# Performance work log

Measured on AMD Instinct MI355X. Metric: run time of the kernel, lower is better.

The kernel has to match this reference:

```python
import jax, jax.numpy as jnp
import numpy as np

N_ITER = 5          # n_iterations
EPS_VAR = 1e-6      # added to var (both in update_likelihoods and after M-step)
EPS = 1e-7          # division guard in M-step


def setup_inputs() -> dict:
    key = jax.random.key(0)
    B, N, K, F = 8, 80000, 5, 20
    k1, k2 = jax.random.split(key)
    data = jax.random.normal(k1, (B, N, F), dtype=jnp.float32)
    # initialize_parameters: means are randomly sampled data points
    idx = jax.random.randint(k2, (B, K), 0, N)
    means = jnp.take_along_axis(data, idx[:, :, None], axis=1)          # [B,K,F]
    variance = jnp.ones((B, K, F), dtype=jnp.float32)                    # covariance_init=1.0
    prior = jnp.full((B, K), 1.0 / K, dtype=jnp.float32)
    return {"data": data, "means": means, "variance": variance, "prior": prior}


def _log_likelihoods(data, means, var, pi):
    # data [B,N,F], means/var [B,K,F], pi [B,K] -> [B,K,N]
    inv_cov = 1.0 / (var + EPS_VAR)                                       # [B,K,F]
    diff = data[:, None, :, :] - means[:, :, None, :]                     # [B,K,N,F]
    maha = jnp.einsum('bknf,bkf->bkn', diff * diff, inv_cov)              # bmm in torch
    coeff = -0.5 * jnp.log(2.0 * np.pi * var).sum(axis=-1)                # [B,K]
    return jnp.log(pi)[:, :, None] + coeff[:, :, None] - 0.5 * maha


def _posteriors(log_lik):
    # stable softmax over the cluster dim (dim=1), identical to update_posteriors
    return jax.nn.softmax(log_lik, axis=1)


def _m_step(post, data):
    # post [B,K,N], data [B,N,F]; weights == 1.0 branch of update_parameters
    n = data.shape[1]
    sizes = post.sum(axis=2, keepdims=True)                               # [B,K,1] cluster sizes
    pi = sizes[..., 0] / n                                                # [B,K]
    pi = pi / jnp.maximum(jnp.abs(pi).sum(axis=-1, keepdims=True), 1e-12) # L1 normalize
    means = jnp.einsum('bkn,bnf->bkf', post, data) / (sizes + EPS)        # [B,K,F]
    diff = data[:, None, :, :] - means[:, :, None, :]                     # [B,K,N,F]
    var = jnp.einsum('bkn,bknf->bkf', post, diff * diff) / (sizes + EPS)
    return means, var, pi


def reference(data, means, variance, prior):
    var, pi = variance, prior
    for _ in range(N_ITER):
        ll = _log_likelihoods(data, means, var, pi)
        post = _posteriors(ll)
        means, var, pi = _m_step(post, data)
        var = var + EPS_VAR
    ll = _log_likelihoods(data, means, var, pi)
    post = _posteriors(ll)
    # outputs permuted to [B, N, K] as in forward()
    return (jnp.transpose(ll, (0, 2, 1)), jnp.transpose(post, (0, 2, 1)), means, var, pi)
```

## Files before the change

kernel.cpp:

```cpp
#include <hip/hip_runtime.h>
#include <math.h>

#define BB 8
#define NPTS 80000
#define KK 5
#define FF 20
#define GG 128
#define TILE 64
#define NTILES (NPTS / TILE)
#define PSTRIDE 48

#define WS_CM 0
#define WS_CV 800
#define WS_CP 1600
#define WS_A  1640
#define WS_D  1680
#define WS_E  2480

__device__ __forceinline__ void make_coefs(const float* __restrict__ means,
                                           const float* __restrict__ var,
                                           const float* __restrict__ pi,
                                           float* __restrict__ A, float* __restrict__ D,
                                           float* __restrict__ E, int t) {
    if (t < BB * KK) {
        float sumlog = 0.f, summ2 = 0.f;
        for (int f = 0; f < FF; ++f) {
            float v = var[t * FF + f];
            float m = means[t * FF + f];
            float ic = 1.f / (v + 1e-6f);
            sumlog += logf(6.283185307179586f * v);
            summ2  += ic * m * m;
            D[t * FF + f] = ic * m;
            E[t * FF + f] = -0.5f * ic;
        }
        A[t] = logf(pi[t]) - 0.5f * sumlog - 0.5f * summ2;
    }
}

__global__ void prepare_kernel(const float* __restrict__ means, const float* __restrict__ var,
                               const float* __restrict__ pi, float* __restrict__ ws) {
    make_coefs(means, var, pi, ws + WS_A, ws + WS_D, ws + WS_E, (int)threadIdx.x);
}

template <bool WRITE_OUT>
__global__ __launch_bounds__(320) void estep_kernel(const float* __restrict__ data,
                                                    const float* __restrict__ ws,
                                                    float* __restrict__ partials,
                                                    float* __restrict__ out_ll,
                                                    float* __restrict__ out_post) {
    __shared__ float xs[FF][TILE + 1];
    __shared__ float lls[KK][TILE];

    const int b    = blockIdx.x / GG;
    const int g    = blockIdx.x % GG;
    const int tid  = threadIdx.x;
    const int w    = __builtin_amdgcn_readfirstlane(tid >> 6);
    const int lane = tid & 63;
    const int sp   = (tid * 4) / FF;
    const int sf   = (tid * 4) % FF;

    const float* A = ws + WS_A;
    const float* D = ws + WS_D;
    const float* E = ws + WS_E;

    const float Ak = A[b * KK + w];
    float dk[FF], ek[FF];
#pragma unroll
    for (int f = 0; f < FF; ++f) {
        dk[f] = D[(b * KK + w) * FF + f];
        ek[f] = E[(b * KK + w) * FF + f];
    }

    float s0 = 0.f, s1[FF], s2[FF];
    if (!WRITE_OUT) {
#pragma unroll
        for (int f = 0; f < FF; ++f) { s1[f] = 0.f; s2[f] = 0.f; }
    }

    const float* dbase = data + (size_t)b * NPTS * FF;

    float4 v = ((const float4*)(dbase + (size_t)g * TILE * FF))[tid];
    for (int t = g; t < NTILES; t += GG) {
        const int tn = t + GG;
        float4 vn = v;
        if (tn < NTILES) vn = ((const float4*)(dbase + (size_t)tn * TILE * FF))[tid];

        xs[sf][sp] = v.x; xs[sf + 1][sp] = v.y; xs[sf + 2][sp] = v.z; xs[sf + 3][sp] = v.w;
        __syncthreads();

        float x[FF];
        float z = Ak;
#pragma unroll
        for (int f = 0; f < FF; ++f) {
            x[f] = xs[f][lane];
            z += x[f] * fmaf(ek[f], x[f], dk[f]);
        }
        lls[w][lane] = z;
        __syncthreads();

        float l0 = lls[0][lane], l1 = lls[1][lane], l2 = lls[2][lane],
              l3 = lls[3][lane], l4 = lls[4][lane];
        float mx = fmaxf(fmaxf(fmaxf(l0, l1), fmaxf(l2, l3)), l4);
        float e0 = __expf(l0 - mx), e1 = __expf(l1 - mx), e2 = __expf(l2 - mx),
              e3 = __expf(l3 - mx), e4 = __expf(l4 - mx);
        float inv = 1.f / (e0 + e1 + e2 + e3 + e4);
        float ew  = (w == 0) ? e0 : (w == 1) ? e1 : (w == 2) ? e2 : (w == 3) ? e3 : e4;
        float post = ew * inv;

        if (WRITE_OUT) {
            size_t o = ((size_t)b * NPTS + (size_t)t * TILE + lane) * KK + w;
            out_ll[o]   = z;
            out_post[o] = post;
        } else {
            s0 += post;
#pragma unroll
            for (int f = 0; f < FF; ++f) {
                float px = post * x[f];
                s1[f] += px;
                s2[f] += px * x[f];
            }
        }
        v = vn;
    }

    if (!WRITE_OUT) {
#pragma unroll
        for (int off = 32; off > 0; off >>= 1) {
            s0 += __shfl_down(s0, off);
#pragma unroll
            for (int f = 0; f < FF; ++f) {
                s1[f] += __shfl_down(s1[f], off);
                s2[f] += __shfl_down(s2[f], off);
            }
        }
        if (lane == 0) {
            float* row = partials + ((size_t)(b * KK + w) * GG + g) * PSTRIDE;
#pragma unroll
            for (int f = 0; f < FF; ++f) { row[f] = s1[f]; row[FF + f] = s2[f]; }
            row[2 * FF] = s0;
        }
    }
}

__global__ __launch_bounds__(320) void update_kernel(const float* __restrict__ partials,
                                                     float* __restrict__ ws,
                                                     float* __restrict__ om,
                                                     float* __restrict__ ov,
                                                     float* __restrict__ op,
                                                     int write_params) {
    __shared__ float s0s[KK];
    const int b    = blockIdx.x;
    const int tid  = threadIdx.x;
    const int w    = tid >> 6;
    const int lane = tid & 63;
    const int bk   = b * KK + w;

    float sv = 0.f;
    if (lane < PSTRIDE) {
        const float* base = partials + (size_t)bk * GG * PSTRIDE + lane;
        for (int gg = 0; gg < GG; ++gg) sv += base[(size_t)gg * PSTRIDE];
    }
    float s0  = __shfl(sv, 2 * FF);
    float den = s0 + 1e-7f;
    float m   = sv / den;
    float s2f = __shfl(sv, FF + (lane % FF));
    float var = (s2f - 2.f * m * sv + m * m * s0) / den + 1e-6f;

    float* cm = ws + WS_CM; float* cv = ws + WS_CV; float* cp = ws + WS_CP;
    if (lane < FF) {
        cm[bk * FF + lane] = m;
        cv[bk * FF + lane] = var;
        if (write_params) { om[bk * FF + lane] = m; ov[bk * FF + lane] = var; }
    }

    if (lane == 0) s0s[w] = s0;
    __syncthreads();
    float tot = s0s[0] + s0s[1] + s0s[2] + s0s[3] + s0s[4];
    float pr  = (s0 / (float)NPTS) / fmaxf(tot / (float)NPTS, 1e-12f);
    if (lane == 0) {
        cp[bk] = pr;
        if (write_params) op[bk] = pr;
    }

    float ic = 1.f / (var + 1e-6f);
    if (lane < FF) {
        (ws + WS_D)[bk * FF + lane] = ic * m;
        (ws + WS_E)[bk * FF + lane] = -0.5f * ic;
    }
    float t1 = (lane < FF) ? logf(6.283185307179586f * var) : 0.f;
    float t2 = (lane < FF) ? ic * m * m : 0.f;
#pragma unroll
    for (int off = 1; off < 64; off <<= 1) {
        t1 += __shfl_xor(t1, off);
        t2 += __shfl_xor(t2, off);
    }
    if (lane == 0)
        (ws + WS_A)[bk] = logf(pr) - 0.5f * t1 - 0.5f * t2;
}

extern "C" void kernel_launch(void* const* d_in, const int* in_sizes, int n_in,
                              void* d_out, int out_size, void* d_ws, size_t ws_size,
                              hipStream_t stream) {
    const float* data     = (const float*)d_in[0];
    const float* in_means = (const float*)d_in[1];
    const float* in_var   = (const float*)d_in[2];
    const float* in_pi    = (const float*)d_in[3];
    float* ws  = (float*)d_ws;
    float* out = (float*)d_out;

    float* out_ll   = out;
    float* out_post = out + (size_t)BB * NPTS * KK;
    float* om       = out + 2 * (size_t)BB * NPTS * KK;
    float* ov       = om + BB * KK * FF;
    float* op       = ov + BB * KK * FF;

    float* partials = out_ll;

    prepare_kernel<<<1, 64, 0, stream>>>(in_means, in_var, in_pi, ws);

    for (int it = 0; it < 5; ++it) {
        estep_kernel<false><<<BB * GG, 320, 0, stream>>>(data, ws, partials,
                                                         nullptr, nullptr);
        update_kernel<<<BB, 320, 0, stream>>>(partials, ws, om, ov, op,
                                              (it == 4) ? 1 : 0);
    }
    estep_kernel<true><<<BB * GG, 320, 0, stream>>>(data, ws, nullptr,
                                                    out_ll, out_post);
}
```

Before: 285.8 us.

## Process two points per lane, double-buffer tiles, parallelize parameter update per cluster

The E-step tile doubles to 128 points, so each lane handles two points per iteration with a double-buffered shared tile, and the grid grows to 192 blocks per batch. The update kernel now launches one block per (batch, cluster) and spreads the partial-sum reduction over four waves plus a separate cluster-size reduction. The aim is to amortize barriers and shared-memory traffic over more points, add memory-level parallelism, and shorten the serial update reduction. In exchange it raises register pressure (with launch bounds asking for 8 blocks) and adds more partial rows to reduce.

Measured after the change: 621.0 us. +117.3%, slower.

```diff
diff --git a/kernel.cpp b/kernel.cpp
--- a/kernel.cpp
+++ b/kernel.cpp
@@ -5,8 +5,8 @@
 #define NPTS 80000
 #define KK 5
 #define FF 20
-#define GG 128
-#define TILE 64
+#define GG 192
+#define TILE 128
 #define NTILES (NPTS / TILE)
 #define PSTRIDE 48
 
@@ -43,12 +43,12 @@
 }
 
 template <bool WRITE_OUT>
-__global__ __launch_bounds__(320) void estep_kernel(const float* __restrict__ data,
-                                                    const float* __restrict__ ws,
-                                                    float* __restrict__ partials,
-                                                    float* __restrict__ out_ll,
-                                                    float* __restrict__ out_post) {
-    __shared__ float xs[FF][TILE + 1];
+__global__ __launch_bounds__(320, 8) void estep_kernel(const float* __restrict__ data,
+                                                       const float* __restrict__ ws,
+                                                       float* __restrict__ partials,
+                                                       float* __restrict__ out_ll,
+                                                       float* __restrict__ out_post) {
+    __shared__ float xs[2][FF][TILE + 1];
     __shared__ float lls[KK][TILE];
 
     const int b    = blockIdx.x / GG;
@@ -56,8 +56,9 @@
     const int tid  = threadIdx.x;
     const int w    = __builtin_amdgcn_readfirstlane(tid >> 6);
     const int lane = tid & 63;
-    const int sp   = (tid * 4) / FF;
-    const int sf   = (tid * 4) % FF;
+    const int fi   = tid * 8;
+    const int sp0  = fi / FF,       sf0 = fi % FF;
+    const int sp1  = (fi + 4) / FF, sf1 = (fi + 4) % FF;
 
     const float* A = ws + WS_A;
     const float* D = ws + WS_D;
@@ -79,48 +80,81 @@
 
     const float* dbase = data + (size_t)b * NPTS * FF;
 
-    float4 v = ((const float4*)(dbase + (size_t)g * TILE * FF))[tid];
+    const float4* tpf = (const float4*)(dbase + (size_t)g * TILE * FF);
+    float4 va = tpf[2 * tid];
+    float4 vb = tpf[2 * tid + 1];
+    int buf = 0;
+
     for (int t = g; t < NTILES; t += GG) {
         const int tn = t + GG;
-        float4 vn = v;
-        if (tn < NTILES) vn = ((const float4*)(dbase + (size_t)tn * TILE * FF))[tid];
-
-        xs[sf][sp] = v.x; xs[sf + 1][sp] = v.y; xs[sf + 2][sp] = v.z; xs[sf + 3][sp] = v.w;
+        float4 na = va, nb = vb;
+        if (tn < NTILES) {
+            const float4* tp = (const float4*)(dbase + (size_t)tn * TILE * FF);
+            na = tp[2 * tid];
+            nb = tp[2 * tid + 1];
+        }
+
+        xs[buf][sf0][sp0]     = va.x;
+        xs[buf][sf0 + 1][sp0] = va.y;
+        xs[buf][sf0 + 2][sp0] = va.z;
+        xs[buf][sf0 + 3][sp0] = va.w;
+        xs[buf][sf1][sp1]     = vb.x;
+        xs[buf][sf1 + 1][sp1] = vb.y;
+        xs[buf][sf1 + 2][sp1] = vb.z;
+        xs[buf][sf1 + 3][sp1] = vb.w;
         __syncthreads();
 
-        float x[FF];
-        float z = Ak;
+        float z0 = Ak, z1 = Ak;
 #pragma unroll
         for (int f = 0; f < FF; ++f) {
-            x[f] = xs[f][lane];
-            z += x[f] * fmaf(ek[f], x[f], dk[f]);
-        }
-        lls[w][lane] = z;
+            float x0 = xs[buf][f][lane];
+            float x1 = xs[buf][f][lane + 64];
+            z0 += x0 * fmaf(ek[f], x0, dk[f]);
+            z1 += x1 * fmaf(ek[f], x1, dk[f]);
+        }
+        lls[w][lane]      = z0;
+        lls[w][lane + 64] = z1;
         __syncthreads();
 
-        float l0 = lls[0][lane], l1 = lls[1][lane], l2 = lls[2][lane],
-              l3 = lls[3][lane], l4 = lls[4][lane];
-        float mx = fmaxf(fmaxf(fmaxf(l0, l1), fmaxf(l2, l3)), l4);
-        float e0 = __expf(l0 - mx), e1 = __expf(l1 - mx), e2 = __expf(l2 - mx),
-              e3 = __expf(l3 - mx), e4 = __expf(l4 - mx);
-        float inv = 1.f / (e0 + e1 + e2 + e3 + e4);
-        float ew  = (w == 0) ? e0 : (w == 1) ? e1 : (w == 2) ? e2 : (w == 3) ? e3 : e4;
-        float post = ew * inv;
+        float a0 = lls[0][lane], a1 = lls[1][lane], a2 = lls[2][lane],
+              a3 = lls[3][lane], a4 = lls[4][lane];
+        float mx0 = fmaxf(fmaxf(fmaxf(a0, a1), fmaxf(a2, a3)), a4);
+        float e0 = __expf(a0 - mx0), e1 = __expf(a1 - mx0), e2 = __expf(a2 - mx0),
+              e3 = __expf(a3 - mx0), e4 = __expf(a4 - mx0);
+        float inv0 = 1.f / (e0 + e1 + e2 + e3 + e4);
+        float ew0  = (w == 0) ? e0 : (w == 1) ? e1 : (w == 2) ? e2 : (w == 3) ? e3 : e4;
+        float post0 = ew0 * inv0;
+
+        float b0 = lls[0][lane + 64], b1 = lls[1][lane + 64], b2 = lls[2][lane + 64],
+              b3 = lls[3][lane + 64], b4 = lls[4][lane + 64];
+        float mx1 = fmaxf(fmaxf(fmaxf(b0, b1), fmaxf(b2, b3)), b4);
+        float f0 = __expf(b0 - mx1), f1 = __expf(b1 - mx1), f2 = __expf(b2 - mx1),
+              f3 = __expf(b3 - mx1), f4 = __expf(b4 - mx1);
+        float inv1 = 1.f / (f0 + f1 + f2 + f3 + f4);
+        float ew1  = (w == 0) ? f0 : (w == 1) ? f1 : (w == 2) ? f2 : (w == 3) ? f3 : f4;
+        float post1 = ew1 * inv1;
 
         if (WRITE_OUT) {
-            size_t o = ((size_t)b * NPTS + (size_t)t * TILE + lane) * KK + w;
-            out_ll[o]   = z;
-            out_post[o] = post;
+            size_t o0 = ((size_t)b * NPTS + (size_t)t * TILE + lane) * KK + w;
+            out_ll[o0]   = z0;
+            out_post[o0] = post0;
+            size_t o1 = o0 + (size_t)64 * KK;
+            out_ll[o1]   = z1;
+            out_post[o1] = post1;
         } else {
-            s0 += post;
+            s0 += post0 + post1;
 #pragma unroll
             for (int f = 0; f < FF; ++f) {
-                float px = post * x[f];
-                s1[f] += px;
-                s2[f] += px * x[f];
+                float x0 = xs[buf][f][lane];
+                float x1 = xs[buf][f][lane + 64];
+                float q0 = post0 * x0;
+                float q1 = post1 * x1;
+                s1[f] += q0 + q1;
+                s2[f] = fmaf(q0, x0, s2[f]);
+                s2[f] = fmaf(q1, x1, s2[f]);
             }
         }
-        v = vn;
+        va = na; vb = nb; buf ^= 1;
     }
 
     if (!WRITE_OUT) {
@@ -142,60 +176,78 @@
     }
 }
 
-__global__ __launch_bounds__(320) void update_kernel(const float* __restrict__ partials,
+__global__ __launch_bounds__(256) void update_kernel(const float* __restrict__ partials,
                                                      float* __restrict__ ws,
                                                      float* __restrict__ om,
                                                      float* __restrict__ ov,
                                                      float* __restrict__ op,
                                                      int write_params) {
-    __shared__ float s0s[KK];
-    const int b    = blockIdx.x;
+    __shared__ float shA[4][PSTRIDE];
+    __shared__ float shB[8 * KK];
+    const int bk   = blockIdx.x;
+    const int b    = bk / KK;
     const int tid  = threadIdx.x;
-    const int w    = tid >> 6;
+    const int w4   = tid >> 6;
     const int lane = tid & 63;
-    const int bk   = b * KK + w;
-
-    float sv = 0.f;
+
     if (lane < PSTRIDE) {
         const float* base = partials + (size_t)bk * GG * PSTRIDE + lane;
-        for (int gg = 0; gg < GG; ++gg) sv += base[(size_t)gg * PSTRIDE];
-    }
-    float s0  = __shfl(sv, 2 * FF);
-    float den = s0 + 1e-7f;
-    float m   = sv / den;
-    float s2f = __shfl(sv, FF + (lane % FF));
-    float var = (s2f - 2.f * m * sv + m * m * s0) / den + 1e-6f;
-
-    float* cm = ws + WS_CM; float* cv = ws + WS_CV; float* cp = ws + WS_CP;
-    if (lane < FF) {
-        cm[bk * FF + lane] = m;
-        cv[bk * FF + lane] = var;
-        if (write_params) { om[bk * FF + lane] = m; ov[bk * FF + lane] = var; }
-    }
-
-    if (lane == 0) s0s[w] = s0;
+        float sv = 0.f;
+        for (int gg = w4; gg < GG; gg += 4) sv += base[(size_t)gg * PSTRIDE];
+        shA[w4][lane] = sv;
+    }
+    if (tid < 8 * KK) {
+        const int kp = tid >> 3, j = tid & 7;
+        const float* cb = partials + (size_t)(b * KK + kp) * GG * PSTRIDE + 2 * FF;
+        float s = 0.f;
+        for (int gg = j; gg < GG; gg += 8) s += cb[(size_t)gg * PSTRIDE];
+        shB[tid] = s;
+    }
     __syncthreads();
-    float tot = s0s[0] + s0s[1] + s0s[2] + s0s[3] + s0s[4];
-    float pr  = (s0 / (float)NPTS) / fmaxf(tot / (float)NPTS, 1e-12f);
-    if (lane == 0) {
-        cp[bk] = pr;
-        if (write_params) op[bk] = pr;
-    }
-
-    float ic = 1.f / (var + 1e-6f);
-    if (lane < FF) {
-        (ws + WS_D)[bk * FF + lane] = ic * m;
-        (ws + WS_E)[bk * FF + lane] = -0.5f * ic;
-    }
-    float t1 = (lane < FF) ? logf(6.283185307179586f * var) : 0.f;
-    float t2 = (lane < FF) ? ic * m * m : 0.f;
-#pragma unroll
-    for (int off = 1; off < 64; off <<= 1) {
-        t1 += __shfl_xor(t1, off);
-        t2 += __shfl_xor(t2, off);
-    }
-    if (lane == 0)
-        (ws + WS_A)[bk] = logf(pr) - 0.5f * t1 - 0.5f * t2;
+
+    if (tid < 64) {
+        float svt = 0.f;
+        if (lane < PSTRIDE)
+            svt = shA[0][lane] + shA[1][lane] + shA[2][lane] + shA[3][lane];
+
+        float tb = (lane < 8 * KK) ? shB[lane] : 0.f;
+#pragma unroll
+        for (int off = 32; off > 0; off >>= 1) tb += __shfl_xor(tb, off);
+
+        float s0  = __shfl(svt, 2 * FF);
+        float den = s0 + 1e-7f;
+        float m   = svt / den;
+        float s2f = __shfl(svt, FF + (lane % FF));
+        float var = (s2f - 2.f * m * svt + m * m * s0) / den + 1e-6f;
+
+        float* cm = ws + WS_CM; float* cv = ws + WS_CV; float* cp = ws + WS_CP;
+        if (lane < FF) {
+            cm[bk * FF + lane] = m;
+            cv[bk * FF + lane] = var;
+            if (write_params) { om[bk * FF + lane] = m; ov[bk * FF + lane] = var; }
+        }
+
+        float pr = (s0 / (float)NPTS) / fmaxf(tb / (float)NPTS, 1e-12f);
+        if (lane == 0) {
+            cp[bk] = pr;
+            if (write_params) op[bk] = pr;
+        }
+
+        float ic = 1.f / (var + 1e-6f);
+        if (lane < FF) {
+            (ws + WS_D)[bk * FF + lane] = ic * m;
+            (ws + WS_E)[bk * FF + lane] = -0.5f * ic;
+        }
+        float t1 = (lane < FF) ? logf(6.283185307179586f * var) : 0.f;
+        float t2 = (lane < FF) ? ic * m * m : 0.f;
+#pragma unroll
+        for (int off = 1; off < 64; off <<= 1) {
+            t1 += __shfl_xor(t1, off);
+            t2 += __shfl_xor(t2, off);
+        }
+        if (lane == 0)
+            (ws + WS_A)[bk] = logf(pr) - 0.5f * t1 - 0.5f * t2;
+    }
 }
 
 extern "C" void kernel_launch(void* const* d_in, const int* in_sizes, int n_in,
@@ -221,8 +273,8 @@
     for (int it = 0; it < 5; ++it) {
         estep_kernel<false><<<BB * GG, 320, 0, stream>>>(data, ws, partials,
                                                          nullptr, nullptr);
-        update_kernel<<<BB, 320, 0, stream>>>(partials, ws, om, ov, op,
-                                              (it == 4) ? 1 : 0);
+        update_kernel<<<BB * KK, 256, 0, stream>>>(partials, ws, om, ov, op,
+                                                   (it == 4) ? 1 : 0);
     }
     estep_kernel<true><<<BB * GG, 320, 0, stream>>>(data, ws, nullptr,
                                                     out_ll, out_post);
```

## Load points directly from global, double-buffer LDS, and parallelize update reduction

Applied to the files above, without the earlier changes.

The E-step drops the shared-memory transpose of the data tile. Each lane now reads its own point's 20 features straight from global memory with five float4 loads, so one of the two block barriers per tile goes away; the log-likelihood exchange buffer is double-buffered and uses a hand-written waitcnt+barrier. A one-element prefetch of the next tile replaces the explicit register double-buffering. The update kernel is split into one block per (batch, cluster) with 8 waves reducing partials in parallel instead of one wave serially summing 128 rows. Risk: every one of the 5 waves re-reads the same data from global/L2 instead of sharing it through LDS, and the per-lane strided loads are less coalesced.

Measured after the change: 327.7 us. +14.7%, slower.

```diff
diff --git a/kernel.cpp b/kernel.cpp
--- a/kernel.cpp
+++ b/kernel.cpp
@@ -16,6 +16,8 @@
 #define WS_A  1640
 #define WS_D  1680
 #define WS_E  2480
+
+#define WAIT_BAR() asm volatile("s_waitcnt lgkmcnt(0)\n\ts_barrier" ::: "memory")
 
 __device__ __forceinline__ void make_coefs(const float* __restrict__ means,
                                            const float* __restrict__ var,
@@ -48,16 +50,13 @@
                                                     float* __restrict__ partials,
                                                     float* __restrict__ out_ll,
                                                     float* __restrict__ out_post) {
-    __shared__ float xs[FF][TILE + 1];
-    __shared__ float lls[KK][TILE];
+    __shared__ float lls[2][KK][TILE];
 
     const int b    = blockIdx.x / GG;
     const int g    = blockIdx.x % GG;
     const int tid  = threadIdx.x;
     const int w    = __builtin_amdgcn_readfirstlane(tid >> 6);
     const int lane = tid & 63;
-    const int sp   = (tid * 4) / FF;
-    const int sf   = (tid * 4) % FF;
 
     const float* A = ws + WS_A;
     const float* D = ws + WS_D;
@@ -78,28 +77,40 @@
     }
 
     const float* dbase = data + (size_t)b * NPTS * FF;
-
-    float4 v = ((const float4*)(dbase + (size_t)g * TILE * FF))[tid];
+    int pb = 0;
+
     for (int t = g; t < NTILES; t += GG) {
+        const float* xp = dbase + ((size_t)t * TILE + lane) * FF;
+        float4 xa = ((const float4*)xp)[0];
+        float4 xb = ((const float4*)xp)[1];
+        float4 xc = ((const float4*)xp)[2];
+        float4 xd = ((const float4*)xp)[3];
+        float4 xe = ((const float4*)xp)[4];
+
+        float pf = 0.f;
         const int tn = t + GG;
-        float4 vn = v;
-        if (tn < NTILES) vn = ((const float4*)(dbase + (size_t)tn * TILE * FF))[tid];
-
-        xs[sf][sp] = v.x; xs[sf + 1][sp] = v.y; xs[sf + 2][sp] = v.z; xs[sf + 3][sp] = v.w;
-        __syncthreads();
+        if (tn < NTILES) pf = dbase[((size_t)tn * TILE + lane) * FF];
 
         float x[FF];
-        float z = Ak;
-#pragma unroll
-        for (int f = 0; f < FF; ++f) {
-            x[f] = xs[f][lane];
-            z += x[f] * fmaf(ek[f], x[f], dk[f]);
-        }
-        lls[w][lane] = z;
-        __syncthreads();
-
-        float l0 = lls[0][lane], l1 = lls[1][lane], l2 = lls[2][lane],
-              l3 = lls[3][lane], l4 = lls[4][lane];
+        x[0]=xa.x; x[1]=xa.y; x[2]=xa.z; x[3]=xa.w;
+        x[4]=xb.x; x[5]=xb.y; x[6]=xb.z; x[7]=xb.w;
+        x[8]=xc.x; x[9]=xc.y; x[10]=xc.z; x[11]=xc.w;
+        x[12]=xd.x; x[13]=xd.y; x[14]=xd.z; x[15]=xd.w;
+        x[16]=xe.x; x[17]=xe.y; x[18]=xe.z; x[19]=xe.w;
+
+        float za = 0.f, zb = 0.f;
+#pragma unroll
+        for (int f = 0; f < FF; f += 2) {
+            za = fmaf(x[f],     fmaf(ek[f],     x[f],     dk[f]),     za);
+            zb = fmaf(x[f + 1], fmaf(ek[f + 1], x[f + 1], dk[f + 1]), zb);
+        }
+        float z = Ak + za + zb;
+
+        lls[pb][w][lane] = z;
+        WAIT_BAR();
+
+        float l0 = lls[pb][0][lane], l1 = lls[pb][1][lane], l2 = lls[pb][2][lane],
+              l3 = lls[pb][3][lane], l4 = lls[pb][4][lane];
         float mx = fmaxf(fmaxf(fmaxf(l0, l1), fmaxf(l2, l3)), l4);
         float e0 = __expf(l0 - mx), e1 = __expf(l1 - mx), e2 = __expf(l2 - mx),
               e3 = __expf(l3 - mx), e4 = __expf(l4 - mx);
@@ -117,10 +128,11 @@
             for (int f = 0; f < FF; ++f) {
                 float px = post * x[f];
                 s1[f] += px;
-                s2[f] += px * x[f];
+                s2[f] = fmaf(px, x[f], s2[f]);
             }
         }
-        v = vn;
+        asm volatile("" :: "v"(pf));
+        pb ^= 1;
     }
 
     if (!WRITE_OUT) {
@@ -142,60 +154,80 @@
     }
 }
 
-__global__ __launch_bounds__(320) void update_kernel(const float* __restrict__ partials,
+__global__ __launch_bounds__(512) void update_kernel(const float* __restrict__ partials,
                                                      float* __restrict__ ws,
                                                      float* __restrict__ om,
                                                      float* __restrict__ ov,
                                                      float* __restrict__ op,
                                                      int write_params) {
-    __shared__ float s0s[KK];
-    const int b    = blockIdx.x;
+    __shared__ float shA[8][PSTRIDE];
+    __shared__ float shB[8 * KK];
+    const int bk   = blockIdx.x;
+    const int b    = bk / KK;
     const int tid  = threadIdx.x;
-    const int w    = tid >> 6;
+    const int w8   = tid >> 6;
     const int lane = tid & 63;
-    const int bk   = b * KK + w;
-
-    float sv = 0.f;
+
     if (lane < PSTRIDE) {
         const float* base = partials + (size_t)bk * GG * PSTRIDE + lane;
-        for (int gg = 0; gg < GG; ++gg) sv += base[(size_t)gg * PSTRIDE];
-    }
-    float s0  = __shfl(sv, 2 * FF);
-    float den = s0 + 1e-7f;
-    float m   = sv / den;
-    float s2f = __shfl(sv, FF + (lane % FF));
-    float var = (s2f - 2.f * m * sv + m * m * s0) / den + 1e-6f;
-
-    float* cm = ws + WS_CM; float* cv = ws + WS_CV; float* cp = ws + WS_CP;
-    if (lane < FF) {
-        cm[bk * FF + lane] = m;
-        cv[bk * FF + lane] = var;
-        if (write_params) { om[bk * FF + lane] = m; ov[bk * FF + lane] = var; }
-    }
-
-    if (lane == 0) s0s[w] = s0;
+        float sv = 0.f;
+        for (int gg = w8; gg < GG; gg += 8) sv += base[(size_t)gg * PSTRIDE];
+        shA[w8][lane] = sv;
+    }
+    if (tid < 8 * KK) {
+        const int kp = tid >> 3, j = tid & 7;
+        const float* cb = partials + (size_t)(b * KK + kp) * GG * PSTRIDE + 2 * FF;
+        float s = 0.f;
+        for (int gg = j; gg < GG; gg += 8) s += cb[(size_t)gg * PSTRIDE];
+        shB[tid] = s;
+    }
     __syncthreads();
-    float tot = s0s[0] + s0s[1] + s0s[2] + s0s[3] + s0s[4];
-    float pr  = (s0 / (float)NPTS) / fmaxf(tot / (float)NPTS, 1e-12f);
-    if (lane == 0) {
-        cp[bk] = pr;
-        if (write_params) op[bk] = pr;
-    }
-
-    float ic = 1.f / (var + 1e-6f);
-    if (lane < FF) {
-        (ws + WS_D)[bk * FF + lane] = ic * m;
-        (ws + WS_E)[bk * FF + lane] = -0.5f * ic;
-    }
-    float t1 = (lane < FF) ? logf(6.283185307179586f * var) : 0.f;
-    float t2 = (lane < FF) ? ic * m * m : 0.f;
-#pragma unroll
-    for (int off = 1; off < 64; off <<= 1) {
-        t1 += __shfl_xor(t1, off);
-        t2 += __shfl_xor(t2, off);
-    }
-    if (lane == 0)
-        (ws + WS_A)[bk] = logf(pr) - 0.5f * t1 - 0.5f * t2;
+
+    if (tid < 64) {
+        float svt = 0.f;
+        if (lane < PSTRIDE) {
+            svt = (shA[0][lane] + shA[1][lane]) + (shA[2][lane] + shA[3][lane])
+                + (shA[4][lane] + shA[5][lane]) + (shA[6][lane] + shA[7][lane]);
+        }
+
+        float tb = (lane < 8 * KK) ? shB[lane] : 0.f;
+#pragma unroll
+        for (int off = 32; off > 0; off >>= 1) tb += __shfl_xor(tb, off);
+
+        float s0  = __shfl(svt, 2 * FF);
+        float den = s0 + 1e-7f;
+        float m   = svt / den;
+        float s2f = __shfl(svt, FF + (lane % FF));
+        float var = (s2f - 2.f * m * svt + m * m * s0) / den + 1e-6f;
+
+        float* cm = ws + WS_CM; float* cv = ws + WS_CV; float* cp = ws + WS_CP;
+        if (lane < FF) {
+            cm[bk * FF + lane] = m;
+            cv[bk * FF + lane] = var;
+            if (write_params) { om[bk * FF + lane] = m; ov[bk * FF + lane] = var; }
+        }
+
+        float pr = (s0 / (float)NPTS) / fmaxf(tb / (float)NPTS, 1e-12f);
+        if (lane == 0) {
+            cp[bk] = pr;
+            if (write_params) op[bk] = pr;
+        }
+
+        float ic = 1.f / (var + 1e-6f);
+        if (lane < FF) {
+            (ws + WS_D)[bk * FF + lane] = ic * m;
+            (ws + WS_E)[bk * FF + lane] = -0.5f * ic;
+        }
+        float t1 = (lane < FF) ? logf(6.283185307179586f * var) : 0.f;
+        float t2 = (lane < FF) ? ic * m * m : 0.f;
+#pragma unroll
+        for (int off = 1; off < 64; off <<= 1) {
+            t1 += __shfl_xor(t1, off);
+            t2 += __shfl_xor(t2, off);
+        }
+        if (lane == 0)
+            (ws + WS_A)[bk] = logf(pr) - 0.5f * t1 - 0.5f * t2;
+    }
 }
 
 extern "C" void kernel_launch(void* const* d_in, const int* in_sizes, int n_in,
@@ -221,8 +253,8 @@
     for (int it = 0; it < 5; ++it) {
         estep_kernel<false><<<BB * GG, 320, 0, stream>>>(data, ws, partials,
                                                          nullptr, nullptr);
-        update_kernel<<<BB, 320, 0, stream>>>(partials, ws, om, ov, op,
-                                              (it == 4) ? 1 : 0);
+        update_kernel<<<BB * KK, 512, 0, stream>>>(partials, ws, om, ov, op,
+                                                   (it == 4) ? 1 : 0);
     }
     estep_kernel<true><<<BB * GG, 320, 0, stream>>>(data, ws, nullptr,
                                                     out_ll, out_post);
```
